# Performance work log

Hardware: AMD Instinct MI355X
Metric: run time of the kernel (lower is better)

## Reference

```python
import jax, jax.numpy as jnp
import numpy as np

N, P, T, K = 20000, 5, 16, 3
IN, H, O = 150, 64, 128


def setup_inputs() -> dict:
    key = jax.random.key(0)
    k1, k2, k3, k4, k5 = jax.random.split(key, 5)
    x = jax.random.normal(k1, (N, IN), dtype=jnp.float32)
    conn_idx = jax.random.randint(k2, (N, P, T, K), 0, N, dtype=jnp.int32)
    conn_w = jax.random.uniform(k3, (N, P, T, K), dtype=jnp.float32)
    # learned params
    W1 = jax.random.normal(k4, (H, IN), dtype=jnp.float32) * 0.05   # linear_1 (no bias)
    Wg = jax.random.normal(k5, (O, H, P, T), dtype=jnp.float32) * 0.05  # geodesic conv weight
    bg = jnp.zeros((O,), dtype=jnp.float32)                          # geodesic conv bias
    return {"x": x, "conn_idx": conn_idx, "conn_w": conn_w, "W1": W1, "Wg": Wg, "bg": bg}


def reference(x, conn_idx, conn_w, W1, Wg, bg):
    # Linear + ReLU: [N, H]
    h = jax.nn.relu(x @ W1.T)
    # Geodesic patch gather: interpolate vertex features into P x T bins
    g = jnp.take(h, conn_idx, axis=0)                 # [N, P, T, K, H]
    patches = jnp.einsum('nptk,nptkh->npth', conn_w, g)  # [N, P, T, H]
    # Geodesic convolution: contract patch bins and channels
    out = jnp.einsum('npth,ohpt->no', patches, Wg) + bg  # [N, O]
    # L2 normalize per vertex
    norm = jnp.linalg.norm(out, axis=-1, keepdims=True)
    return out / norm
```

## Files before the change

kernel.cpp:

```cpp
#include <hip/hip_runtime.h>
#include <hip/hip_fp16.h>

#define NV   20000
#define KK   3
#define INF  150
#define HH   64
#define OO   128
#define PT   80
#define KTOT 5120
#define NB   32
#define BS   72
#define HRS  296
#define HALF (NB * HRS)
#define XS   168

typedef _Float16 fh8 __attribute__((ext_vector_type(8)));
typedef __attribute__((ext_vector_type(4))) float f32x4;

__device__ __forceinline__ unsigned short f2h(float f) {
    return __half_as_ushort(__float2half(f));
}

struct Conn { int idx[12]; float w[12]; };

__global__ __launch_bounds__(256) void prep_kernel(
    const float* __restrict__ Wg, const float* __restrict__ x,
    const float* __restrict__ W1, unsigned short* __restrict__ W2,
    unsigned short* __restrict__ hb) {
    __shared__ __align__(16) unsigned char smem[32256];
    const int tid = threadIdx.x;

    if (blockIdx.x < 128) {
        float* lds = (float*)smem;
        const int o = blockIdx.x;
        const float* src = Wg + o * KTOT;
        for (int t = tid; t < KTOT; t += 256) {
            int h = t / 80, bin = t - h * 80;
            lds[h * 81 + bin] = src[t];
        }
        __syncthreads();
        for (int t = tid; t < KTOT; t += 256) {
            W2[(t >> 5) * 4096 + o * 32 + (t & 31)] =
                f2h(lds[(t & 63) * 81 + (t >> 6)]);
        }
        return;
    }

    unsigned short* xs = (unsigned short*)smem;
    unsigned short* ws = xs + 32 * XS;
    const int n0 = (blockIdx.x - 128) * 32;

    for (int e = tid; e < 32 * INF; e += 256) {
        int r = e / INF, c = e - r * INF;
        xs[r * XS + c] = f2h(x[n0 * INF + e]);
    }
    for (int e = tid; e < 32 * 18; e += 256) {
        int r = e / 18, c = e - r * 18;
        xs[r * XS + 150 + c] = 0;
    }
    for (int e = tid; e < 64 * INF; e += 256) {
        int r = e / INF, c = e - r * INF;
        ws[r * XS + c] = f2h(W1[e]);
    }
    for (int e = tid; e < 64 * 18; e += 256) {
        int r = e / 18, c = e - r * 18;
        ws[r * XS + 150 + c] = 0;
    }
    __syncthreads();

    const int wv   = tid >> 6;
    const int lane = tid & 63;
    const int q    = lane >> 4;
    const int r16  = lane & 15;
    const int o0   = wv * 16;

    f32x4 acc0 = {0.f, 0.f, 0.f, 0.f};
    f32x4 acc1 = acc0;
    #pragma unroll
    for (int s = 0; s < 5; s++) {
        const int kb = s * 32 + q * 8;
        fh8 a0 = *(const fh8*)(xs + r16 * XS + kb);
        fh8 a1 = *(const fh8*)(xs + (16 + r16) * XS + kb);
        fh8 b  = *(const fh8*)(ws + (o0 + r16) * XS + kb);
        acc0 = __builtin_amdgcn_mfma_f32_16x16x32_f16(a0, b, acc0, 0, 0, 0);
        acc1 = __builtin_amdgcn_mfma_f32_16x16x32_f16(a1, b, acc1, 0, 0, 0);
    }
    #pragma unroll
    for (int r = 0; r < 4; r++) {
        float v0 = acc0[r] > 0.f ? acc0[r] : 0.f;
        float v1 = acc1[r] > 0.f ? acc1[r] : 0.f;
        hb[(n0 + q * 4 + r) * HH + o0 + r16]      = f2h(v0);
        hb[(n0 + 16 + q * 4 + r) * HH + o0 + r16] = f2h(v1);
    }
}

__global__ __launch_bounds__(256, 2) void geo_kernel(
    const int*   __restrict__ conn_idx, const float* __restrict__ conn_w,
    const unsigned short* __restrict__ W2, const unsigned short* __restrict__ hb,
    const float* __restrict__ bg, float* __restrict__ out) {
    __shared__ __align__(16) unsigned short pch[2 * HALF];
    __shared__ float rsq[NB];
    float* outbuf = (float*)pch;

    const int tid  = threadIdx.x;
    const int n0   = blockIdx.x * NB;
    const int wv   = tid >> 6;
    const int lane = tid & 63;
    const int q    = lane >> 4;
    const int r16  = lane & 15;
    const int j8   = tid & 7;
    const int bb   = (tid >> 3) & 3;
    const int nb8  = tid >> 5;

    f32x4 acc00 = {0.f, 0.f, 0.f, 0.f};
    f32x4 acc01 = acc00, acc10 = acc00, acc11 = acc00;

    Conn cA, cB;
    fh8  hv[12];

    auto loadc = [&](int hc, Conn& c) {
        #pragma unroll
        for (int i = 0; i < 4; i++) {
            const int n = i * 8 + nb8;
            const int g = (n0 + n) * (PT * KK) + (hc * 4 + bb) * KK;
            c.idx[i * 3 + 0] = conn_idx[g];
            c.idx[i * 3 + 1] = conn_idx[g + 1];
            c.idx[i * 3 + 2] = conn_idx[g + 2];
            c.w[i * 3 + 0]   = conn_w[g];
            c.w[i * 3 + 1]   = conn_w[g + 1];
            c.w[i * 3 + 2]   = conn_w[g + 2];
        }
    };
    auto loadh = [&](const Conn& c) {
        #pragma unroll
        for (int t = 0; t < 12; t++)
            hv[t] = *(const fh8*)(hb + c.idx[t] * HH + j8 * 8);
    };
    auto cwrite = [&](const Conn& c, unsigned short* buf) {
        #pragma unroll
        for (int i = 0; i < 4; i++) {
            const int n = i * 8 + nb8;
            _Float16 w0 = (_Float16)c.w[i * 3 + 0];
            _Float16 w1 = (_Float16)c.w[i * 3 + 1];
            _Float16 w2 = (_Float16)c.w[i * 3 + 2];
            fh8 W0 = {w0, w0, w0, w0, w0, w0, w0, w0};
            fh8 W1v = {w1, w1, w1, w1, w1, w1, w1, w1};
            fh8 W2v = {w2, w2, w2, w2, w2, w2, w2, w2};
            fh8 r = hv[i * 3] * W0 + hv[i * 3 + 1] * W1v + hv[i * 3 + 2] * W2v;
            *(fh8*)(buf + n * HRS + bb * BS + j8 * 8) = r;
        }
    };
    auto mfmaph = [&](const unsigned short* buf, int hc) {
        #pragma unroll
        for (int s = 0; s < 8; s++) {
            const int S  = hc * 8 + s;
            const int ao = (s >> 1) * BS + (s & 1) * 32 + q * 8;
            fh8 a0 = *(const fh8*)(buf + r16 * HRS + ao);
            fh8 a1 = *(const fh8*)(buf + (16 + r16) * HRS + ao);
            fh8 b0 = *(const fh8*)(W2 + S * 4096 + (wv * 32 + r16) * 32 + q * 8);
            fh8 b1 = *(const fh8*)(W2 + S * 4096 + (wv * 32 + 16 + r16) * 32 + q * 8);
            acc00 = __builtin_amdgcn_mfma_f32_16x16x32_f16(a0, b0, acc00, 0, 0, 0);
            acc01 = __builtin_amdgcn_mfma_f32_16x16x32_f16(a0, b1, acc01, 0, 0, 0);
            acc10 = __builtin_amdgcn_mfma_f32_16x16x32_f16(a1, b0, acc10, 0, 0, 0);
            acc11 = __builtin_amdgcn_mfma_f32_16x16x32_f16(a1, b1, acc11, 0, 0, 0);
        }
    };

    loadc(0, cA);
    loadc(1, cB);
    loadh(cA);
    cwrite(cA, pch);
    __syncthreads();

    auto body = [&](int hc, Conn& use, Conn& fill) {
        if (hc + 2 < 20) loadc(hc + 2, fill);
        if (hc + 1 < 20) loadh(use);
        mfmaph(&pch[(hc & 1) * HALF], hc);
        if (hc + 1 < 20) cwrite(use, &pch[((hc + 1) & 1) * HALF]);
        __syncthreads();
    };
    for (int hc = 0; hc < 20; hc += 2) {
        body(hc, cB, cA);
        body(hc + 1, cA, cB);
    }

    {
        const int o0 = wv * 32;
        #pragma unroll
        for (int r = 0; r < 4; r++) {
            outbuf[(q * 4 + r) * 132 + o0 + r16]           = acc00[r];
            outbuf[(q * 4 + r) * 132 + o0 + 16 + r16]      = acc01[r];
            outbuf[(16 + q * 4 + r) * 132 + o0 + r16]      = acc10[r];
            outbuf[(16 + q * 4 + r) * 132 + o0 + 16 + r16] = acc11[r];
        }
    }
    __syncthreads();
    {
        int rr = tid >> 3, l = tid & 7;
        float s = 0.f;
        for (int o = l; o < 128; o += 8) {
            float v = outbuf[rr * 132 + o] + bg[o];
            s += v * v;
        }
        for (int off = 4; off; off >>= 1) s += __shfl_down(s, off, 8);
        if (l == 0) rsq[rr] = rsqrtf(s);
    }
    __syncthreads();
    #pragma unroll
    for (int i = 0; i < 16; i++) {
        int e = i * 256 + tid;
        int n = e >> 7, o = e & 127;
        out[(n0 + n) * OO + o] = (outbuf[n * 132 + o] + bg[o]) * rsq[n];
    }
}

extern "C" void kernel_launch(void* const* d_in, const int* in_sizes, int n_in,
                              void* d_out, int out_size, void* d_ws, size_t ws_size,
                              hipStream_t stream) {
    const float* x        = (const float*)d_in[0];
    const int*   conn_idx = (const int*)  d_in[1];
    const float* conn_w   = (const float*)d_in[2];
    const float* W1       = (const float*)d_in[3];
    const float* Wg       = (const float*)d_in[4];
    const float* bg       = (const float*)d_in[5];
    float*       out      = (float*)d_out;

    unsigned short* W2 = (unsigned short*)d_ws;
    unsigned short* hb = W2 + OO * KTOT;

    hipLaunchKernelGGL(prep_kernel, dim3(128 + NV / 32), dim3(256), 0, stream,
                       Wg, x, W1, W2, hb);
    hipLaunchKernelGGL(geo_kernel, dim3(NV / NB), dim3(256), 0, stream,
                       conn_idx, conn_w, W2, hb, bg, out);
}
```

Before: 195.4 us.

## Split geodesic reduction across two blocks per tile and add normalize kernel

The 80-bin contraction is split in half (split-K): each 32-vertex tile now gets two blocks, each handling 40 bins with half the shared memory. One half writes fp32 partial sums to the output and the other writes fp16 partials to workspace. A third kernel then adds the partials and bias and L2-normalizes. This doubles grid parallelism and raises occupancy (launch bounds 4) to hide gather latency. The cost is an extra launch, extra global round-trips for the partials, and lower precision in the second partial.

```diff
diff --git a/kernel.cpp b/kernel.cpp
--- a/kernel.cpp
+++ b/kernel.cpp
@@ -9,9 +9,9 @@
 #define PT   80
 #define KTOT 5120
 #define NB   32
-#define BS   72
-#define HRS  296
-#define HALF (NB * HRS)
+#define BS2  72
+#define RS2  152
+#define CHB  (NB * RS2)
 #define XS   168
 
 typedef _Float16 fh8 __attribute__((ext_vector_type(8)));
@@ -20,8 +20,11 @@
 __device__ __forceinline__ unsigned short f2h(float f) {
     return __half_as_ushort(__float2half(f));
 }
-
-struct Conn { int idx[12]; float w[12]; };
+__device__ __forceinline__ float h2f(unsigned short u) {
+    return __half2float(__ushort_as_half(u));
+}
+
+struct Conn { int idx[6]; float w[6]; };
 
 __global__ __launch_bounds__(256) void prep_kernel(
     const float* __restrict__ Wg, const float* __restrict__ x,
@@ -94,35 +97,36 @@
     }
 }
 
-__global__ __launch_bounds__(256, 2) void geo_kernel(
+__global__ __launch_bounds__(256, 4) void geo_kernel(
     const int*   __restrict__ conn_idx, const float* __restrict__ conn_w,
     const unsigned short* __restrict__ W2, const unsigned short* __restrict__ hb,
-    const float* __restrict__ bg, float* __restrict__ out) {
-    __shared__ __align__(16) unsigned short pch[2 * HALF];
-    __shared__ float rsq[NB];
-    float* outbuf = (float*)pch;
+    float* __restrict__ out, unsigned short* __restrict__ part1) {
+    __shared__ __align__(16) unsigned short pch[2 * CHB];
 
     const int tid  = threadIdx.x;
-    const int n0   = blockIdx.x * NB;
+    const int ks   = blockIdx.x & 1;
+    const int n0   = (blockIdx.x >> 1) * NB;
     const int wv   = tid >> 6;
     const int lane = tid & 63;
     const int q    = lane >> 4;
     const int r16  = lane & 15;
     const int j8   = tid & 7;
-    const int bb   = (tid >> 3) & 3;
-    const int nb8  = tid >> 5;
+    const int bl   = (tid >> 3) & 1;
+    const int ng   = tid >> 4;
+    const int bbase = ks * 40;
+    const int Sbase = ks * 80;
 
     f32x4 acc00 = {0.f, 0.f, 0.f, 0.f};
     f32x4 acc01 = acc00, acc10 = acc00, acc11 = acc00;
 
     Conn cA, cB;
-    fh8  hv[12];
-
-    auto loadc = [&](int hc, Conn& c) {
-        #pragma unroll
-        for (int i = 0; i < 4; i++) {
-            const int n = i * 8 + nb8;
-            const int g = (n0 + n) * (PT * KK) + (hc * 4 + bb) * KK;
+    fh8  hv[6];
+
+    auto loadc = [&](int cc, Conn& c) {
+        const int bin = bbase + cc * 2 + bl;
+        #pragma unroll
+        for (int i = 0; i < 2; i++) {
+            const int g = (n0 + ng + i * 16) * (PT * KK) + bin * KK;
             c.idx[i * 3 + 0] = conn_idx[g];
             c.idx[i * 3 + 1] = conn_idx[g + 1];
             c.idx[i * 3 + 2] = conn_idx[g + 2];
@@ -133,13 +137,13 @@
     };
     auto loadh = [&](const Conn& c) {
         #pragma unroll
-        for (int t = 0; t < 12; t++)
+        for (int t = 0; t < 6; t++)
             hv[t] = *(const fh8*)(hb + c.idx[t] * HH + j8 * 8);
     };
     auto cwrite = [&](const Conn& c, unsigned short* buf) {
         #pragma unroll
-        for (int i = 0; i < 4; i++) {
-            const int n = i * 8 + nb8;
+        for (int i = 0; i < 2; i++) {
+            const int n = ng + i * 16;
             _Float16 w0 = (_Float16)c.w[i * 3 + 0];
             _Float16 w1 = (_Float16)c.w[i * 3 + 1];
             _Float16 w2 = (_Float16)c.w[i * 3 + 2];
@@ -147,16 +151,16 @@
             fh8 W1v = {w1, w1, w1, w1, w1, w1, w1, w1};
             fh8 W2v = {w2, w2, w2, w2, w2, w2, w2, w2};
             fh8 r = hv[i * 3] * W0 + hv[i * 3 + 1] * W1v + hv[i * 3 + 2] * W2v;
-            *(fh8*)(buf + n * HRS + bb * BS + j8 * 8) = r;
-        }
-    };
-    auto mfmaph = [&](const unsigned short* buf, int hc) {
-        #pragma unroll
-        for (int s = 0; s < 8; s++) {
-            const int S  = hc * 8 + s;
-            const int ao = (s >> 1) * BS + (s & 1) * 32 + q * 8;
-            fh8 a0 = *(const fh8*)(buf + r16 * HRS + ao);
-            fh8 a1 = *(const fh8*)(buf + (16 + r16) * HRS + ao);
+            *(fh8*)(buf + n * RS2 + bl * BS2 + j8 * 8) = r;
+        }
+    };
+    auto mfmaph = [&](const unsigned short* buf, int cc) {
+        #pragma unroll
+        for (int s = 0; s < 4; s++) {
+            const int S  = Sbase + cc * 4 + s;
+            const int ao = (s >> 1) * BS2 + (s & 1) * 32 + q * 8;
+            fh8 a0 = *(const fh8*)(buf + r16 * RS2 + ao);
+            fh8 a1 = *(const fh8*)(buf + (16 + r16) * RS2 + ao);
             fh8 b0 = *(const fh8*)(W2 + S * 4096 + (wv * 32 + r16) * 32 + q * 8);
             fh8 b1 = *(const fh8*)(W2 + S * 4096 + (wv * 32 + 16 + r16) * 32 + q * 8);
             acc00 = __builtin_amdgcn_mfma_f32_16x16x32_f16(a0, b0, acc00, 0, 0, 0);
@@ -172,46 +176,57 @@
     cwrite(cA, pch);
     __syncthreads();
 
-    auto body = [&](int hc, Conn& use, Conn& fill) {
-        if (hc + 2 < 20) loadc(hc + 2, fill);
-        if (hc + 1 < 20) loadh(use);
-        mfmaph(&pch[(hc & 1) * HALF], hc);
-        if (hc + 1 < 20) cwrite(use, &pch[((hc + 1) & 1) * HALF]);
+    auto body = [&](int cc, Conn& use, Conn& fill) {
+        if (cc + 2 < 20) loadc(cc + 2, fill);
+        if (cc + 1 < 20) loadh(use);
+        mfmaph(&pch[(cc & 1) * CHB], cc);
+        if (cc + 1 < 20) cwrite(use, &pch[((cc + 1) & 1) * CHB]);
         __syncthreads();
     };
-    for (int hc = 0; hc < 20; hc += 2) {
-        body(hc, cB, cA);
-        body(hc + 1, cA, cB);
-    }
-
-    {
-        const int o0 = wv * 32;
+    for (int cc = 0; cc < 20; cc += 2) {
+        body(cc, cB, cA);
+        body(cc + 1, cA, cB);
+    }
+
+    const int o0 = wv * 32;
+    if (ks == 0) {
         #pragma unroll
         for (int r = 0; r < 4; r++) {
-            outbuf[(q * 4 + r) * 132 + o0 + r16]           = acc00[r];
-            outbuf[(q * 4 + r) * 132 + o0 + 16 + r16]      = acc01[r];
-            outbuf[(16 + q * 4 + r) * 132 + o0 + r16]      = acc10[r];
-            outbuf[(16 + q * 4 + r) * 132 + o0 + 16 + r16] = acc11[r];
-        }
-    }
-    __syncthreads();
-    {
-        int rr = tid >> 3, l = tid & 7;
-        float s = 0.f;
-        for (int o = l; o < 128; o += 8) {
-            float v = outbuf[rr * 132 + o] + bg[o];
-            s += v * v;
-        }
-        for (int off = 4; off; off >>= 1) s += __shfl_down(s, off, 8);
-        if (l == 0) rsq[rr] = rsqrtf(s);
-    }
-    __syncthreads();
+            out[(n0 + q * 4 + r) * OO + o0 + r16]           = acc00[r];
+            out[(n0 + q * 4 + r) * OO + o0 + 16 + r16]      = acc01[r];
+            out[(n0 + 16 + q * 4 + r) * OO + o0 + r16]      = acc10[r];
+            out[(n0 + 16 + q * 4 + r) * OO + o0 + 16 + r16] = acc11[r];
+        }
+    } else {
+        #pragma unroll
+        for (int r = 0; r < 4; r++) {
+            part1[(n0 + q * 4 + r) * OO + o0 + r16]           = f2h(acc00[r]);
+            part1[(n0 + q * 4 + r) * OO + o0 + 16 + r16]      = f2h(acc01[r]);
+            part1[(n0 + 16 + q * 4 + r) * OO + o0 + r16]      = f2h(acc10[r]);
+            part1[(n0 + 16 + q * 4 + r) * OO + o0 + 16 + r16] = f2h(acc11[r]);
+        }
+    }
+}
+
+__global__ __launch_bounds__(256) void norm_kernel(
+    float* __restrict__ out, const unsigned short* __restrict__ part1,
+    const float* __restrict__ bg) {
+    const int tid = threadIdx.x;
+    const int n   = blockIdx.x * 32 + (tid >> 3);
+    const int l   = tid & 7;
+    float v[16];
+    float s = 0.f;
     #pragma unroll
     for (int i = 0; i < 16; i++) {
-        int e = i * 256 + tid;
-        int n = e >> 7, o = e & 127;
-        out[(n0 + n) * OO + o] = (outbuf[n * 132 + o] + bg[o]) * rsq[n];
-    }
+        const int o = i * 8 + l;
+        v[i] = out[n * OO + o] + h2f(part1[n * OO + o]) + bg[o];
+        s += v[i] * v[i];
+    }
+    for (int off = 4; off; off >>= 1) s += __shfl_down(s, off, 8);
+    const float r = rsqrtf(__shfl(s, 0, 8));
+    #pragma unroll
+    for (int i = 0; i < 16; i++)
+        out[n * OO + i * 8 + l] = v[i] * r;
 }
 
 extern "C" void kernel_launch(void* const* d_in, const int* in_sizes, int n_in,
@@ -225,11 +240,14 @@
     const float* bg       = (const float*)d_in[5];
     float*       out      = (float*)d_out;
 
-    unsigned short* W2 = (unsigned short*)d_ws;
-    unsigned short* hb = W2 + OO * KTOT;
+    unsigned short* W2    = (unsigned short*)d_ws;
+    unsigned short* hb    = W2 + OO * KTOT;
+    unsigned short* part1 = hb + NV * HH;
 
     hipLaunchKernelGGL(prep_kernel, dim3(128 + NV / 32), dim3(256), 0, stream,
                        Wg, x, W1, W2, hb);
-    hipLaunchKernelGGL(geo_kernel, dim3(NV / NB), dim3(256), 0, stream,
-                       conn_idx, conn_w, W2, hb, bg, out);
-}
+    hipLaunchKernelGGL(geo_kernel, dim3(2 * NV / NB), dim3(256), 0, stream,
+                       conn_idx, conn_w, W2, hb, out, part1);
+    hipLaunchKernelGGL(norm_kernel, dim3(NV / 32), dim3(256), 0, stream,
+                       out, part1, bg);
+}
```

Measured after the change: 188.6 us. 1.04x faster.
